# Kernel tuning notes

Hardware: AMD Instinct MI355X
Metric: run time of the kernel (lower is better)

Reference implementation:

```python
import jax, jax.numpy as jnp
import numpy as np

N_NODES = 100_000
N_EDGES = 800_000
HIDDEN = 150
EDGE_FEAT = 7
N_LAYERS = 4
N_GRAPHS = 128
OUT_DIM = 6
BN_EPS = 1e-5


def setup_inputs() -> dict:
    key = jax.random.key(0)
    ks = jax.random.split(key, 16)
    x = jnp.zeros((N_NODES,), dtype=jnp.int32)  # Embedding(1, D) -> all indices 0
    edge_index = jax.random.randint(ks[0], (2, N_EDGES), 0, N_NODES, dtype=jnp.int32)
    edge_attr = jax.random.normal(ks[1], (N_EDGES, EDGE_FEAT), dtype=jnp.float32)
    batch = jnp.sort(jax.random.randint(ks[2], (N_NODES,), 0, N_GRAPHS, dtype=jnp.int32))
    s = 0.05
    node_emb = jax.random.normal(ks[3], (1, HIDDEN), dtype=jnp.float32) * s
    Wl = jax.random.normal(ks[4], (N_LAYERS, HIDDEN, HIDDEN), dtype=jnp.float32) * s
    bl = jnp.zeros((N_LAYERS, HIDDEN), dtype=jnp.float32)
    We = jax.random.normal(ks[5], (N_LAYERS, EDGE_FEAT, HIDDEN), dtype=jnp.float32) * s
    be = jnp.zeros((N_LAYERS, HIDDEN), dtype=jnp.float32)
    root = jax.random.normal(ks[6], (N_LAYERS, 1, HIDDEN), dtype=jnp.float32) * s
    gamma = jnp.ones((N_LAYERS, HIDDEN), dtype=jnp.float32)
    beta = jnp.zeros((N_LAYERS, HIDDEN), dtype=jnp.float32)
    Wp = jax.random.normal(ks[7], (HIDDEN, OUT_DIM), dtype=jnp.float32) * s
    bp = jnp.zeros((OUT_DIM,), dtype=jnp.float32)
    return {"x": x, "edge_index": edge_index, "edge_attr": edge_attr, "batch": batch,
            "node_emb": node_emb, "Wl": Wl, "bl": bl, "We": We, "be": be,
            "root": root, "gamma": gamma, "beta": beta, "Wp": Wp, "bp": bp}


def reference(x, edge_index, edge_attr, batch, node_emb, Wl, bl, We, be, root, gamma, beta, Wp, bp):
    n = x.shape[0]
    row, col = edge_index[0], edge_index[1]  # j=source, i=target (PyG default flow)
    # degree over row (as in GCNConv.forward), +1
    deg = jax.ops.segment_sum(jnp.ones((row.shape[0],), edge_attr.dtype), row, num_segments=n) + 1.0
    dis = deg ** -0.5  # deg >= 1, no inf
    norm = dis[row] * dis[col]  # [E]

    h = node_emb[x]  # [N, D]
    for l in range(N_LAYERS):
        xl = h @ Wl[l] + bl[l]                      # linear
        e = edge_attr @ We[l] + be[l]               # edge encoder
        msg = norm[:, None] * jax.nn.relu(xl[row] + e)      # per-edge message [E, D]
        agg = jax.ops.segment_sum(msg, col, num_segments=n)  # scatter-add to targets
        out = agg + jax.nn.relu(xl + root[l]) / deg[:, None]
        # BatchNorm1d (training-mode batch statistics; dropout disabled = eval)
        mu = out.mean(axis=0)
        var = out.var(axis=0)
        out = gamma[l] * (out - mu) * jax.lax.rsqrt(var + BN_EPS) + beta[l]
        if l < N_LAYERS - 1:
            out = jax.nn.relu(out)
        h = out + h  # residual=True

    # global mean pool over graphs
    counts = jax.ops.segment_sum(jnp.ones((n,), h.dtype), batch, num_segments=N_GRAPHS)
    hg = jax.ops.segment_sum(h, batch, num_segments=N_GRAPHS) / jnp.maximum(counts, 1.0)[:, None]
    return hg @ Wp + bp  # [G, OUT_DIM]
```

## Files before the change

kernel.cpp:

```cpp
#include <hip/hip_runtime.h>

#define HID 150
#define LD  160
#define NN  100000
#define NNP 100096
#define NE  800000
#define NG  128
#define NL  4
#define ODIM 6
#define BN_EPS 1e-5f
#define NSLICE 32
#define NB_SCAN 98

typedef __attribute__((ext_vector_type(8))) short short8;
typedef __attribute__((ext_vector_type(4))) float f32x4;
typedef unsigned short ushort_t;

__device__ __forceinline__ unsigned short f2bf(float f) {
    union { float f; unsigned int u; } v; v.f = f;
    unsigned int u = v.u;
    unsigned int r = (u + 0x7FFFu + ((u >> 16) & 1u)) >> 16;
    return (unsigned short)r;
}
__device__ __forceinline__ float bf2f(unsigned short h) {
    union { unsigned int u; float f; } v; v.u = ((unsigned int)h) << 16;
    return v.f;
}

__global__ __launch_bounds__(256) void k_deg_count(const int* __restrict__ erow,
                                                   const int* __restrict__ ecol,
                                                   int* __restrict__ degi,
                                                   int* __restrict__ indeg) {
    int e = blockIdx.x * 256 + threadIdx.x;
    if (e < NE) {
        atomicAdd(&degi[erow[e]], 1);
        atomicAdd(&indeg[ecol[e]], 1);
    }
}

__global__ __launch_bounds__(256) void k_deg_fin(const int* __restrict__ degi,
                                                 float* __restrict__ degf,
                                                 float* __restrict__ dis) {
    int n = blockIdx.x * 256 + threadIdx.x;
    if (n < NN) {
        float dg = (float)degi[n] + 1.0f;
        degf[n] = dg;
        dis[n] = rsqrtf(dg);
    }
}

__global__ __launch_bounds__(1024) void k_scanA(const int* __restrict__ in,
                                                int* __restrict__ part,
                                                int* __restrict__ btot) {
    const int tid = threadIdx.x;
    const int lane = tid & 63, wave = tid >> 6;
    const int i = blockIdx.x * 1024 + tid;
    int v = (i < NN) ? in[i] : 0;
    int x = v;
#pragma unroll
    for (int o = 1; o < 64; o <<= 1) {
        int t = __shfl_up(x, o);
        if (lane >= o) x += t;
    }
    __shared__ int wsum[16];
    __shared__ int blocktot;
    if (lane == 63) wsum[wave] = x;
    __syncthreads();
    if (tid < 16) {
        int t = wsum[tid];
        int y = t;
#pragma unroll
        for (int o = 1; o < 16; o <<= 1) {
            int u = __shfl_up(y, o);
            if (tid >= o) y += u;
        }
        wsum[tid] = y - t;
        if (tid == 15) blocktot = y;
    }
    __syncthreads();
    int excl = x - v + wsum[wave];
    if (i < NN) part[i] = excl;
    if (tid == 0) btot[blockIdx.x] = blocktot;
}

__global__ __launch_bounds__(128) void k_scanB(int* __restrict__ btot) {
    const int tid = threadIdx.x;
    const int lane = tid & 63;
    int v = (tid < NB_SCAN) ? btot[tid] : 0;
    int x = v;
#pragma unroll
    for (int o = 1; o < 64; o <<= 1) {
        int t = __shfl_up(x, o);
        if (lane >= o) x += t;
    }
    __shared__ int w2;
    if (tid == 63) w2 = x;
    __syncthreads();
    int ex = x - v + ((tid >= 64) ? w2 : 0);
    if (tid < NB_SCAN) btot[tid] = ex;
}

__global__ __launch_bounds__(256) void k_scanC(int* __restrict__ coff,
                                               const int* __restrict__ btot,
                                               int* __restrict__ cursor) {
    int i = blockIdx.x * 256 + threadIdx.x;
    if (i < NN) {
        int v = coff[i] + btot[i >> 10];
        coff[i] = v;
        cursor[i] = v;
    }
    if (i == 0) coff[NN] = NE;
}

__global__ __launch_bounds__(256) void k_csr_fill(const int* __restrict__ erow,
                                                  const int* __restrict__ ecol,
                                                  const float* __restrict__ ea,
                                                  const float* __restrict__ dis,
                                                  int* __restrict__ cursor,
                                                  int2* __restrict__ csrn,
                                                  uint4* __restrict__ ceab) {
    int e = blockIdx.x * 256 + threadIdx.x;
    if (e >= NE) return;
    const int c = ecol[e], r = erow[e];
    const int p = atomicAdd(&cursor[c], 1);
    int2 m; m.x = r; m.y = __float_as_int(dis[r] * dis[c]);
    csrn[p] = m;
    const float a0 = ea[e * 7 + 0], a1 = ea[e * 7 + 1], a2 = ea[e * 7 + 2],
                a3 = ea[e * 7 + 3], a4 = ea[e * 7 + 4], a5 = ea[e * 7 + 5],
                a6 = ea[e * 7 + 6];
    uint4 A;
    A.x = (unsigned)f2bf(a0) | ((unsigned)f2bf(a1) << 16);
    A.y = (unsigned)f2bf(a2) | ((unsigned)f2bf(a3) << 16);
    A.z = (unsigned)f2bf(a4) | ((unsigned)f2bf(a5) << 16);
    A.w = (unsigned)f2bf(a6);
    ceab[p] = A;
}

__global__ __launch_bounds__(256) void k_wpack(const float* __restrict__ Wl,
                                               unsigned short* __restrict__ Wp) {
    int t = blockIdx.x * 256 + threadIdx.x;
    if (t >= 12800) return;
    const int lane = t & 63;
    const int ct = (t >> 6) % 10;
    const int ks = ((t >> 6) / 10) % 5;
    const int l = t / (64 * 10 * 5);
    const int col = ct * 16 + (lane & 15);
    const int kbase = ks * 32 + (lane >> 4) * 8;
    unsigned short v[8];
#pragma unroll
    for (int j = 0; j < 8; ++j) {
        const int k = kbase + j;
        const float f = (k < HID && col < HID) ? Wl[(size_t)l * HID * HID + k * HID + col] : 0.f;
        v[j] = f2bf(f);
    }
    *(uint4*)(Wp + (size_t)t * 8) = *(const uint4*)v;
}

__global__ __launch_bounds__(256) void k_init_h(const int* __restrict__ x,
                                                const float* __restrict__ emb,
                                                float* __restrict__ h,
                                                unsigned short* __restrict__ hb) {
    int idx = blockIdx.x * 256 + threadIdx.x;
    if (idx >= NNP * LD) return;
    int n = idx / LD;
    int d = idx - n * LD;
    float v = 0.f;
    if (n < NN && d < HID) v = emb[x[n] * HID + d];
    h[idx] = v;
    hb[idx] = f2bf(v);
}

__global__ __launch_bounds__(256) void k_gemm(const unsigned short* __restrict__ hb,
                                              const unsigned short* __restrict__ Wp,
                                              const float* __restrict__ bias,
                                              unsigned short* __restrict__ xlb) {
    __shared__ unsigned short Bs[5 * 10 * 64 * 8];
    {
        const uint4* src = (const uint4*)Wp;
        uint4* dst = (uint4*)Bs;
        for (int i = threadIdx.x; i < 3200; i += 256) dst[i] = src[i];
    }
    __syncthreads();

    const int wave = threadIdx.x >> 6;
    const int lane = threadIdx.x & 63;
    const int row0 = (blockIdx.x * 4 + wave) * 16;
    const int rlo = lane & 15;
    const int khi = lane >> 4;

    short8 a[5];
    {
        const unsigned short* ap = hb + (size_t)(row0 + rlo) * LD + khi * 8;
#pragma unroll
        for (int ks = 0; ks < 5; ++ks)
            a[ks] = *(const short8*)(ap + ks * 32);
    }

    f32x4 acc[10];
#pragma unroll
    for (int ct = 0; ct < 10; ++ct) acc[ct] = (f32x4){0.f, 0.f, 0.f, 0.f};

    const short8* bs = (const short8*)Bs;
#pragma unroll
    for (int ks = 0; ks < 5; ++ks) {
#pragma unroll
        for (int ct = 0; ct < 10; ++ct) {
            acc[ct] = __builtin_amdgcn_mfma_f32_16x16x32_bf16(
                a[ks], bs[(ks * 10 + ct) * 64 + lane], acc[ct], 0, 0, 0);
        }
    }

#pragma unroll
    for (int ct = 0; ct < 10; ++ct) {
        const int col = ct * 16 + rlo;
        if (col < HID) {
            const float b = bias[col];
#pragma unroll
            for (int jj = 0; jj < 4; ++jj) {
                const int row = row0 + khi * 4 + jj;
                xlb[(size_t)row * LD + col] = f2bf(acc[ct][jj] + b);
            }
        }
    }
}

__device__ __forceinline__ float edge_term(const uint4 A, const float w[8]) {
    float ed = w[7];
    ed = fmaf(bf2f((unsigned short)(A.x & 0xffffu)), w[0], ed);
    ed = fmaf(bf2f((unsigned short)(A.x >> 16)), w[1], ed);
    ed = fmaf(bf2f((unsigned short)(A.y & 0xffffu)), w[2], ed);
    ed = fmaf(bf2f((unsigned short)(A.y >> 16)), w[3], ed);
    ed = fmaf(bf2f((unsigned short)(A.z & 0xffffu)), w[4], ed);
    ed = fmaf(bf2f((unsigned short)(A.z >> 16)), w[5], ed);
    ed = fmaf(bf2f((unsigned short)(A.w & 0xffffu)), w[6], ed);
    return ed;
}

__global__ __launch_bounds__(256) void k_agg(const int* __restrict__ coff,
                                             const int2* __restrict__ csrn,
                                             const uint4* __restrict__ ceab,
                                             const float* __restrict__ We,
                                             const float* __restrict__ be,
                                             const float* __restrict__ root,
                                             const float* __restrict__ degf,
                                             const unsigned short* __restrict__ xlb,
                                             float* __restrict__ out,
                                             float* __restrict__ sums) {
    const int lane = threadIdx.x & 63;
    const int gw = (blockIdx.x * 256 + threadIdx.x) >> 6;
    const int nw = (gridDim.x * 256) >> 6;
    const bool ok2 = lane < (HID - 128);
    const int d0 = lane, d1 = lane + 64;
    const int d2 = ok2 ? (lane + 128) : 0;

    float w0[8], w1[8], w2[8];
    float rt0, rt1, rt2;
    {
        const int dd2 = ok2 ? (lane + 128) : 0;
#pragma unroll
        for (int k = 0; k < 7; ++k) {
            w0[k] = We[k * HID + d0];
            w1[k] = We[k * HID + d1];
            w2[k] = ok2 ? We[k * HID + dd2] : 0.f;
        }
        w0[7] = be[d0]; w1[7] = be[d1]; w2[7] = ok2 ? be[dd2] : 0.f;
        rt0 = root[d0]; rt1 = root[d1]; rt2 = ok2 ? root[dd2] : 0.f;
    }

    float s0 = 0.f, s1 = 0.f, s2 = 0.f, q0 = 0.f, q1 = 0.f, q2 = 0.f;

#define ACC_EDGE(m, A, xa, xb, xc)                                        \
    do {                                                                  \
        const float nrm = __int_as_float((m).y);                          \
        acc0 += nrm * fmaxf(bf2f(xa) + edge_term((A), w0), 0.f);          \
        acc1 += nrm * fmaxf(bf2f(xb) + edge_term((A), w1), 0.f);          \
        if (ok2) acc2 += nrm * fmaxf(bf2f(xc) + edge_term((A), w2), 0.f); \
    } while (0)

    for (int i = gw; i < NN; i += nw) {
        const int j1 = coff[i + 1];
        int j = coff[i];
        float acc0 = 0.f, acc1 = 0.f, acc2 = 0.f;
        for (; j + 4 <= j1; j += 4) {
            const int2 m0 = csrn[j], m1 = csrn[j + 1], m2 = csrn[j + 2], m3 = csrn[j + 3];
            const uint4 A0 = ceab[j], A1 = ceab[j + 1], A2 = ceab[j + 2], A3 = ceab[j + 3];
            const unsigned short* p0 = xlb + (size_t)m0.x * LD;
            const unsigned short* p1 = xlb + (size_t)m1.x * LD;
            const unsigned short* p2 = xlb + (size_t)m2.x * LD;
            const unsigned short* p3 = xlb + (size_t)m3.x * LD;
            const unsigned short x0a = p0[d0], x0b = p0[d1], x0c = p0[d2];
            const unsigned short x1a = p1[d0], x1b = p1[d1], x1c = p1[d2];
            const unsigned short x2a = p2[d0], x2b = p2[d1], x2c = p2[d2];
            const unsigned short x3a = p3[d0], x3b = p3[d1], x3c = p3[d2];
            ACC_EDGE(m0, A0, x0a, x0b, x0c);
            ACC_EDGE(m1, A1, x1a, x1b, x1c);
            ACC_EDGE(m2, A2, x2a, x2b, x2c);
            ACC_EDGE(m3, A3, x3a, x3b, x3c);
        }
        for (; j < j1; ++j) {
            const int2 m0 = csrn[j];
            const uint4 A0 = ceab[j];
            const unsigned short* p0 = xlb + (size_t)m0.x * LD;
            const unsigned short x0a = p0[d0], x0b = p0[d1], x0c = p0[d2];
            ACC_EDGE(m0, A0, x0a, x0b, x0c);
        }

        const float inv = 1.0f / degf[i];
        const unsigned short* xi = xlb + (size_t)i * LD;
        float* op = out + (size_t)i * LD;
        {
            const float o = acc0 + fmaxf(bf2f(xi[d0]) + rt0, 0.f) * inv;
            op[d0] = o; s0 += o; q0 += o * o;
        }
        {
            const float o = acc1 + fmaxf(bf2f(xi[d1]) + rt1, 0.f) * inv;
            op[d1] = o; s1 += o; q1 += o * o;
        }
        if (ok2) {
            const float o = acc2 + fmaxf(bf2f(xi[d2]) + rt2, 0.f) * inv;
            op[d2] = o; s2 += o; q2 += o * o;
        }
    }
#undef ACC_EDGE

    __shared__ float ls[2 * LD];
    for (int i = threadIdx.x; i < 2 * LD; i += 256) ls[i] = 0.f;
    __syncthreads();
    atomicAdd(&ls[d0], s0);
    atomicAdd(&ls[LD + d0], q0);
    atomicAdd(&ls[d1], s1);
    atomicAdd(&ls[LD + d1], q1);
    if (ok2) {
        atomicAdd(&ls[d2], s2);
        atomicAdd(&ls[LD + d2], q2);
    }
    __syncthreads();
    float* sl = sums + (size_t)(blockIdx.x & (NSLICE - 1)) * 2 * LD;
    for (int i = threadIdx.x; i < 2 * LD; i += 256) atomicAdd(&sl[i], ls[i]);
}

__global__ void k_stats(const float* __restrict__ sums, const float* __restrict__ gamma,
                        const float* __restrict__ beta, float* __restrict__ ss) {
    int d = threadIdx.x;
    if (d < HID) {
        float s = 0.f, q = 0.f;
        for (int r = 0; r < NSLICE; ++r) {
            s += sums[r * 2 * LD + d];
            q += sums[r * 2 * LD + LD + d];
        }
        const float mu = s * (1.0f / NN);
        const float var = q * (1.0f / NN) - mu * mu;
        const float inv = rsqrtf(var + BN_EPS);
        const float sc = gamma[d] * inv;
        ss[d] = sc;
        ss[LD + d] = beta[d] - mu * sc;
    }
}

__global__ __launch_bounds__(256) void k_apply(const float* __restrict__ out,
                                               const float* __restrict__ ss,
                                               float* __restrict__ h,
                                               unsigned short* __restrict__ hb,
                                               int doRelu) {
    const int lane = threadIdx.x & 63;
    const int gw = (blockIdx.x * 256 + threadIdx.x) >> 6;
    const int nw = (gridDim.x * 256) >> 6;
    const bool ok2 = lane < (HID - 128);

    float sc[3], sh[3];
#pragma unroll
    for (int c = 0; c < 3; ++c) {
        const int d = c * 64 + lane;
        const bool ok = (c < 2) || ok2;
        const int dd = ok ? d : 0;
        sc[c] = ok ? ss[dd] : 0.f;
        sh[c] = ok ? ss[LD + dd] : 0.f;
    }

    for (int n = gw; n < NN; n += nw) {
        float* hp = h + (size_t)n * LD;
        unsigned short* hbp = hb + (size_t)n * LD;
        const float* op = out + (size_t)n * LD;
#pragma unroll
        for (int c = 0; c < 3; ++c) {
            const int d = c * 64 + lane;
            if ((c < 2) || ok2) {
                float o = op[d] * sc[c] + sh[c];
                if (doRelu) o = fmaxf(o, 0.f);
                const float hn = hp[d] + o;
                hp[d] = hn;
                hbp[d] = f2bf(hn);
            }
        }
    }
}

__global__ __launch_bounds__(256) void k_off(const int* __restrict__ batch,
                                             int* __restrict__ off) {
    int n = blockIdx.x * 256 + threadIdx.x;
    if (n >= NN) return;
    int b = batch[n];
    if (n == 0) {
        for (int g = 0; g <= b; ++g) off[g] = 0;
    } else {
        int pb = batch[n - 1];
        for (int g = pb + 1; g <= b; ++g) off[g] = n;
    }
    if (n == NN - 1) {
        for (int g = b + 1; g <= NG; ++g) off[g] = NN;
    }
}

__global__ __launch_bounds__(256) void k_pool(const float* __restrict__ h,
                                              const int* __restrict__ off,
                                              const float* __restrict__ Wp,
                                              const float* __restrict__ bp,
                                              float* __restrict__ out) {
    const int g = blockIdx.x;
    const int s = off[g], e = off[g + 1];
    const float cnt = fmaxf((float)(e - s), 1.0f);
    const int lane = threadIdx.x & 63;
    const int wave = threadIdx.x >> 6;

    float sum[3] = {0.f, 0.f, 0.f};
    for (int n = s + wave; n < e; n += 4) {
        const float* hp = h + (size_t)n * LD;
#pragma unroll
        for (int c = 0; c < 3; ++c) {
            const int d = c * 64 + lane;
            if (d < HID) sum[c] += hp[d];
        }
    }

    __shared__ float hg[LD];
    if (threadIdx.x < LD) hg[threadIdx.x] = 0.f;
    __syncthreads();
#pragma unroll
    for (int c = 0; c < 3; ++c) {
        const int d = c * 64 + lane;
        if (d < HID) atomicAdd(&hg[d], sum[c]);
    }
    __syncthreads();

    if (wave == 0) {
        float acc[ODIM] = {0.f, 0.f, 0.f, 0.f, 0.f, 0.f};
#pragma unroll
        for (int c = 0; c < 3; ++c) {
            const int d = c * 64 + lane;
            if (d < HID) {
                const float v = hg[d] / cnt;
#pragma unroll
                for (int o = 0; o < ODIM; ++o) acc[o] = fmaf(v, Wp[d * ODIM + o], acc[o]);
            }
        }
#pragma unroll
        for (int o = 0; o < ODIM; ++o) {
            float v = acc[o];
            for (int sh = 32; sh > 0; sh >>= 1) v += __shfl_down(v, sh);
            if (lane == 0) out[g * ODIM + o] = v + bp[o];
        }
    }
}

extern "C" void kernel_launch(void* const* d_in, const int* in_sizes, int n_in,
                              void* d_out, int out_size, void* d_ws, size_t ws_size,
                              hipStream_t stream) {
    const int* x = (const int*)d_in[0];
    const int* ei = (const int*)d_in[1];
    const float* ea = (const float*)d_in[2];
    const int* batch = (const int*)d_in[3];
    const float* emb = (const float*)d_in[4];
    const float* Wl = (const float*)d_in[5];
    const float* bl = (const float*)d_in[6];
    const float* We = (const float*)d_in[7];
    const float* be = (const float*)d_in[8];
    const float* root = (const float*)d_in[9];
    const float* gamma = (const float*)d_in[10];
    const float* beta = (const float*)d_in[11];
    const float* Wp = (const float*)d_in[12];
    const float* bp = (const float*)d_in[13];
    float* out = (float*)d_out;

    const int* erow = ei;
    const int* ecol = ei + NE;

    char* ws = (char*)d_ws;
    const size_t SZ4 = (size_t)NNP * LD * 4;
    const size_t SZ2 = (size_t)NNP * LD * 2;
    float* h    = (float*)(ws);
    float* obuf = (float*)(ws + SZ4);
    unsigned short* hb  = (unsigned short*)(ws + 2 * SZ4);
    unsigned short* xlb = (unsigned short*)(ws + 2 * SZ4 + SZ2);
    unsigned short* wpk = (unsigned short*)(ws + 2 * SZ4 + 2 * SZ2);
    char* base = ws + 2 * SZ4 + 2 * SZ2 + 204800;
    int*   degi   = (int*)(base);
    int*   indeg  = (int*)(base + 409600);
    float* degf   = (float*)(base + 819200);
    float* dis    = (float*)(base + 1228800);
    int*   coff   = (int*)(base + 1638400);
    int*   cursor = (int*)(base + 2048000);
    int*   btot   = (int*)(base + 2457600);
    float* sums   = (float*)(base + 2461696);
    float* ssb    = (float*)(base + 2502656);
    int*   goff   = (int*)(base + 2506752);
    int2*  csrn   = (int2*)(base + 2510848);
    uint4* ceab   = (uint4*)(base + 8910848);

    hipMemsetAsync(degi, 0, NN * sizeof(int), stream);
    hipMemsetAsync(indeg, 0, NN * sizeof(int), stream);
    k_deg_count<<<(NE + 255) / 256, 256, 0, stream>>>(erow, ecol, degi, indeg);
    k_deg_fin<<<(NN + 255) / 256, 256, 0, stream>>>(degi, degf, dis);
    k_scanA<<<NB_SCAN, 1024, 0, stream>>>(indeg, coff, btot);
    k_scanB<<<1, 128, 0, stream>>>(btot);
    k_scanC<<<(NN + 255) / 256, 256, 0, stream>>>(coff, btot, cursor);
    k_csr_fill<<<(NE + 255) / 256, 256, 0, stream>>>(erow, ecol, ea, dis, cursor,
                                                     csrn, ceab);
    k_wpack<<<50, 256, 0, stream>>>(Wl, wpk);
    k_init_h<<<(NNP * LD + 255) / 256, 256, 0, stream>>>(x, emb, h, hb);

    for (int l = 0; l < NL; ++l) {
        const float* b_l = bl + (size_t)l * HID;
        const float* We_l = We + (size_t)l * 7 * HID;
        const float* be_l = be + (size_t)l * HID;
        const float* root_l = root + (size_t)l * HID;
        const float* gamma_l = gamma + (size_t)l * HID;
        const float* beta_l = beta + (size_t)l * HID;
        const unsigned short* wpk_l = wpk + (size_t)l * 25600;

        k_gemm<<<NNP / 64, 256, 0, stream>>>(hb, wpk_l, b_l, xlb);
        hipMemsetAsync(sums, 0, NSLICE * 2 * LD * sizeof(float), stream);
        k_agg<<<2048, 256, 0, stream>>>(coff, csrn, ceab, We_l, be_l,
                                        root_l, degf, xlb, obuf, sums);
        k_stats<<<1, 256, 0, stream>>>(sums, gamma_l, beta_l, ssb);
        k_apply<<<2048, 256, 0, stream>>>(obuf, ssb, h, hb, (l < NL - 1) ? 1 : 0);
    }

    k_off<<<(NN + 255) / 256, 256, 0, stream>>>(batch, goff);
    k_pool<<<NG, 256, 0, stream>>>(h, goff, Wp, bp, out);
}
```

Measured before the change: 996.8 us.

## Fuse BN apply and residual into next GEMM and pool; use bf16 dot2 for edge term

Removes the separate k_apply pass and the bf16 copy of h. The next layer's GEMM now reads obuf and h, applies the BN scale/shift, ReLU and residual, writes h back, and converts to bf16 in registers. The last layer's BN and residual are folded into the pooling kernel. The edge-encoder term in aggregation now uses packed bf16 weights with fdot2 instructions instead of seven scalar FMAs, which lowers the precision of the edge weights. The GEMM prologue now reads fp32 data (more bytes per row), and pooling runs with 512 threads.

```diff
diff --git a/kernel.cpp b/kernel.cpp
--- a/kernel.cpp
+++ b/kernel.cpp
@@ -14,7 +14,6 @@
 
 typedef __attribute__((ext_vector_type(8))) short short8;
 typedef __attribute__((ext_vector_type(4))) float f32x4;
-typedef unsigned short ushort_t;
 
 __device__ __forceinline__ unsigned short f2bf(float f) {
     union { float f; unsigned int u; } v; v.f = f;
@@ -25,6 +24,25 @@
 __device__ __forceinline__ float bf2f(unsigned short h) {
     union { unsigned int u; float f; } v; v.u = ((unsigned int)h) << 16;
     return v.f;
+}
+
+#if defined(__has_builtin)
+#if __has_builtin(__builtin_amdgcn_fdot2_f32_bf16)
+#define HAS_DOT2BF 1
+#endif
+#endif
+#ifdef HAS_DOT2BF
+typedef __attribute__((ext_vector_type(2))) __bf16 bf16x2;
+#endif
+__device__ __forceinline__ float dot2bf(unsigned int a, unsigned int b, float c) {
+#ifdef HAS_DOT2BF
+    union { unsigned int u; bf16x2 v; } ua, ub;
+    ua.u = a; ub.u = b;
+    return __builtin_amdgcn_fdot2_f32_bf16(ua.v, ub.v, c, false);
+#else
+    return fmaf(bf2f((unsigned short)(a & 0xffffu)), bf2f((unsigned short)(b & 0xffffu)),
+           fmaf(bf2f((unsigned short)(a >> 16)), bf2f((unsigned short)(b >> 16)), c));
+#endif
 }
 
 __global__ __launch_bounds__(256) void k_deg_count(const int* __restrict__ erow,
@@ -158,8 +176,7 @@
 
 __global__ __launch_bounds__(256) void k_init_h(const int* __restrict__ x,
                                                 const float* __restrict__ emb,
-                                                float* __restrict__ h,
-                                                unsigned short* __restrict__ hb) {
+                                                float* __restrict__ h) {
     int idx = blockIdx.x * 256 + threadIdx.x;
     if (idx >= NNP * LD) return;
     int n = idx / LD;
@@ -167,13 +184,15 @@
     float v = 0.f;
     if (n < NN && d < HID) v = emb[x[n] * HID + d];
     h[idx] = v;
-    hb[idx] = f2bf(v);
-}
-
-__global__ __launch_bounds__(256) void k_gemm(const unsigned short* __restrict__ hb,
+}
+
+__global__ __launch_bounds__(256) void k_gemm(float* __restrict__ h,
+                                              const float* __restrict__ obuf,
+                                              const float* __restrict__ ssb,
                                               const unsigned short* __restrict__ Wp,
                                               const float* __restrict__ bias,
-                                              unsigned short* __restrict__ xlb) {
+                                              unsigned short* __restrict__ xlb,
+                                              int fuse) {
     __shared__ unsigned short Bs[5 * 10 * 64 * 8];
     {
         const uint4* src = (const uint4*)Wp;
@@ -187,13 +206,58 @@
     const int row0 = (blockIdx.x * 4 + wave) * 16;
     const int rlo = lane & 15;
     const int khi = lane >> 4;
+    const int row = row0 + rlo;
+    const bool rowok = row < NN;
 
     short8 a[5];
-    {
-        const unsigned short* ap = hb + (size_t)(row0 + rlo) * LD + khi * 8;
-#pragma unroll
-        for (int ks = 0; ks < 5; ++ks)
-            a[ks] = *(const short8*)(ap + ks * 32);
+    if (fuse) {
+#pragma unroll
+        for (int ks = 0; ks < 5; ++ks) {
+            const int kf = ks * 32 + khi * 8;
+            const size_t base = (size_t)row * LD + kf;
+            const float4 o0 = *(const float4*)(obuf + base);
+            const float4 o1 = *(const float4*)(obuf + base + 4);
+            const float4 h0 = *(const float4*)(h + base);
+            const float4 h1 = *(const float4*)(h + base + 4);
+            const float4 s0 = *(const float4*)(ssb + kf);
+            const float4 s1 = *(const float4*)(ssb + kf + 4);
+            const float4 t0 = *(const float4*)(ssb + LD + kf);
+            const float4 t1 = *(const float4*)(ssb + LD + kf + 4);
+            float hv[8];
+#pragma unroll
+            for (int j = 0; j < 4; ++j) {
+                const bool ok = rowok && (kf + j < HID);
+                hv[j] = ok ? ((&h0.x)[j] + fmaxf((&o0.x)[j] * (&s0.x)[j] + (&t0.x)[j], 0.f)) : 0.f;
+            }
+#pragma unroll
+            for (int j = 0; j < 4; ++j) {
+                const bool ok = rowok && (kf + 4 + j < HID);
+                hv[4 + j] = ok ? ((&h1.x)[j] + fmaxf((&o1.x)[j] * (&s1.x)[j] + (&t1.x)[j], 0.f)) : 0.f;
+            }
+            float4 w0, w1;
+            w0.x = hv[0]; w0.y = hv[1]; w0.z = hv[2]; w0.w = hv[3];
+            w1.x = hv[4]; w1.y = hv[5]; w1.z = hv[6]; w1.w = hv[7];
+            *(float4*)(h + base) = w0;
+            *(float4*)(h + base + 4) = w1;
+            short8 av;
+#pragma unroll
+            for (int j = 0; j < 8; ++j) av[j] = (short)f2bf(hv[j]);
+            a[ks] = av;
+        }
+    } else {
+#pragma unroll
+        for (int ks = 0; ks < 5; ++ks) {
+            const int kf = ks * 32 + khi * 8;
+            const size_t base = (size_t)row * LD + kf;
+            const float4 h0 = *(const float4*)(h + base);
+            const float4 h1 = *(const float4*)(h + base + 4);
+            short8 av;
+#pragma unroll
+            for (int j = 0; j < 4; ++j) av[j] = (short)f2bf((&h0.x)[j]);
+#pragma unroll
+            for (int j = 0; j < 4; ++j) av[4 + j] = (short)f2bf((&h1.x)[j]);
+            a[ks] = av;
+        }
     }
 
     f32x4 acc[10];
@@ -217,23 +281,11 @@
             const float b = bias[col];
 #pragma unroll
             for (int jj = 0; jj < 4; ++jj) {
-                const int row = row0 + khi * 4 + jj;
-                xlb[(size_t)row * LD + col] = f2bf(acc[ct][jj] + b);
+                const int orow = row0 + khi * 4 + jj;
+                xlb[(size_t)orow * LD + col] = f2bf(acc[ct][jj] + b);
             }
         }
     }
-}
-
-__device__ __forceinline__ float edge_term(const uint4 A, const float w[8]) {
-    float ed = w[7];
-    ed = fmaf(bf2f((unsigned short)(A.x & 0xffffu)), w[0], ed);
-    ed = fmaf(bf2f((unsigned short)(A.x >> 16)), w[1], ed);
-    ed = fmaf(bf2f((unsigned short)(A.y & 0xffffu)), w[2], ed);
-    ed = fmaf(bf2f((unsigned short)(A.y >> 16)), w[3], ed);
-    ed = fmaf(bf2f((unsigned short)(A.z & 0xffffu)), w[4], ed);
-    ed = fmaf(bf2f((unsigned short)(A.z >> 16)), w[5], ed);
-    ed = fmaf(bf2f((unsigned short)(A.w & 0xffffu)), w[6], ed);
-    return ed;
 }
 
 __global__ __launch_bounds__(256) void k_agg(const int* __restrict__ coff,
@@ -253,28 +305,38 @@
     const int d0 = lane, d1 = lane + 64;
     const int d2 = ok2 ? (lane + 128) : 0;
 
-    float w0[8], w1[8], w2[8];
-    float rt0, rt1, rt2;
+    unsigned int wp0[4], wp1[4], wp2[4];
+    float be0, be1, be2, rt0, rt1, rt2;
     {
-        const int dd2 = ok2 ? (lane + 128) : 0;
-#pragma unroll
-        for (int k = 0; k < 7; ++k) {
-            w0[k] = We[k * HID + d0];
-            w1[k] = We[k * HID + d1];
-            w2[k] = ok2 ? We[k * HID + dd2] : 0.f;
-        }
-        w0[7] = be[d0]; w1[7] = be[d1]; w2[7] = ok2 ? be[dd2] : 0.f;
-        rt0 = root[d0]; rt1 = root[d1]; rt2 = ok2 ? root[dd2] : 0.f;
+#pragma unroll
+        for (int p = 0; p < 3; ++p) {
+            wp0[p] = (unsigned)f2bf(We[(2 * p) * HID + d0]) | ((unsigned)f2bf(We[(2 * p + 1) * HID + d0]) << 16);
+            wp1[p] = (unsigned)f2bf(We[(2 * p) * HID + d1]) | ((unsigned)f2bf(We[(2 * p + 1) * HID + d1]) << 16);
+            wp2[p] = ok2 ? ((unsigned)f2bf(We[(2 * p) * HID + d2]) | ((unsigned)f2bf(We[(2 * p + 1) * HID + d2]) << 16)) : 0u;
+        }
+        wp0[3] = (unsigned)f2bf(We[6 * HID + d0]);
+        wp1[3] = (unsigned)f2bf(We[6 * HID + d1]);
+        wp2[3] = ok2 ? (unsigned)f2bf(We[6 * HID + d2]) : 0u;
+        be0 = be[d0]; be1 = be[d1]; be2 = ok2 ? be[d2] : 0.f;
+        rt0 = root[d0]; rt1 = root[d1]; rt2 = ok2 ? root[d2] : 0.f;
     }
 
     float s0 = 0.f, s1 = 0.f, s2 = 0.f, q0 = 0.f, q1 = 0.f, q2 = 0.f;
 
-#define ACC_EDGE(m, A, xa, xb, xc)                                        \
-    do {                                                                  \
-        const float nrm = __int_as_float((m).y);                          \
-        acc0 += nrm * fmaxf(bf2f(xa) + edge_term((A), w0), 0.f);          \
-        acc1 += nrm * fmaxf(bf2f(xb) + edge_term((A), w1), 0.f);          \
-        if (ok2) acc2 += nrm * fmaxf(bf2f(xc) + edge_term((A), w2), 0.f); \
+#define ACC_EDGE(m, A, xa, xb, xc)                                                          \
+    do {                                                                                    \
+        const float nrm = __int_as_float((m).y);                                            \
+        const float e0 = dot2bf((A).x, wp0[0], dot2bf((A).y, wp0[1],                        \
+                         dot2bf((A).z, wp0[2], dot2bf((A).w, wp0[3], be0))));               \
+        const float e1 = dot2bf((A).x, wp1[0], dot2bf((A).y, wp1[1],                        \
+                         dot2bf((A).z, wp1[2], dot2bf((A).w, wp1[3], be1))));               \
+        acc0 += nrm * fmaxf(bf2f(xa) + e0, 0.f);                                            \
+        acc1 += nrm * fmaxf(bf2f(xb) + e1, 0.f);                                            \
+        if (ok2) {                                                                          \
+            const float e2 = dot2bf((A).x, wp2[0], dot2bf((A).y, wp2[1],                    \
+                             dot2bf((A).z, wp2[2], dot2bf((A).w, wp2[3], be2))));           \
+            acc2 += nrm * fmaxf(bf2f(xc) + e2, 0.f);                                        \
+        }                                                                                   \
     } while (0)
 
     for (int i = gw; i < NN; i += nw) {
@@ -354,44 +416,9 @@
         const float sc = gamma[d] * inv;
         ss[d] = sc;
         ss[LD + d] = beta[d] - mu * sc;
-    }
-}
-
-__global__ __launch_bounds__(256) void k_apply(const float* __restrict__ out,
-                                               const float* __restrict__ ss,
-                                               float* __restrict__ h,
-                                               unsigned short* __restrict__ hb,
-                                               int doRelu) {
-    const int lane = threadIdx.x & 63;
-    const int gw = (blockIdx.x * 256 + threadIdx.x) >> 6;
-    const int nw = (gridDim.x * 256) >> 6;
-    const bool ok2 = lane < (HID - 128);
-
-    float sc[3], sh[3];
-#pragma unroll
-    for (int c = 0; c < 3; ++c) {
-        const int d = c * 64 + lane;
-        const bool ok = (c < 2) || ok2;
-        const int dd = ok ? d : 0;
-        sc[c] = ok ? ss[dd] : 0.f;
-        sh[c] = ok ? ss[LD + dd] : 0.f;
-    }
-
-    for (int n = gw; n < NN; n += nw) {
-        float* hp = h + (size_t)n * LD;
-        unsigned short* hbp = hb + (size_t)n * LD;
-        const float* op = out + (size_t)n * LD;
-#pragma unroll
-        for (int c = 0; c < 3; ++c) {
-            const int d = c * 64 + lane;
-            if ((c < 2) || ok2) {
-                float o = op[d] * sc[c] + sh[c];
-                if (doRelu) o = fmaxf(o, 0.f);
-                const float hn = hp[d] + o;
-                hp[d] = hn;
-                hbp[d] = f2bf(hn);
-            }
-        }
+    } else if (d < LD) {
+        ss[d] = 0.f;
+        ss[LD + d] = 0.f;
     }
 }
 
@@ -411,7 +438,9 @@
     }
 }
 
-__global__ __launch_bounds__(256) void k_pool(const float* __restrict__ h,
+__global__ __launch_bounds__(512) void k_pool(const float* __restrict__ h,
+                                              const float* __restrict__ obuf,
+                                              const float* __restrict__ ssb,
                                               const int* __restrict__ off,
                                               const float* __restrict__ Wp,
                                               const float* __restrict__ bp,
@@ -421,25 +450,28 @@
     const float cnt = fmaxf((float)(e - s), 1.0f);
     const int lane = threadIdx.x & 63;
     const int wave = threadIdx.x >> 6;
-
-    float sum[3] = {0.f, 0.f, 0.f};
-    for (int n = s + wave; n < e; n += 4) {
+    const bool ok2 = lane < (HID - 128);
+    const int d0 = lane, d1 = lane + 64;
+    const int d2 = ok2 ? (lane + 128) : 0;
+
+    const float sc0 = ssb[d0], sc1 = ssb[d1], sc2 = ok2 ? ssb[d2] : 0.f;
+    const float sh0 = ssb[LD + d0], sh1 = ssb[LD + d1], sh2 = ok2 ? ssb[LD + d2] : 0.f;
+
+    float sum0 = 0.f, sum1 = 0.f, sum2 = 0.f;
+    for (int n = s + wave; n < e; n += 8) {
         const float* hp = h + (size_t)n * LD;
-#pragma unroll
-        for (int c = 0; c < 3; ++c) {
-            const int d = c * 64 + lane;
-            if (d < HID) sum[c] += hp[d];
-        }
+        const float* op = obuf + (size_t)n * LD;
+        sum0 += hp[d0] + (op[d0] * sc0 + sh0);
+        sum1 += hp[d1] + (op[d1] * sc1 + sh1);
+        if (ok2) sum2 += hp[d2] + (op[d2] * sc2 + sh2);
     }
 
     __shared__ float hg[LD];
     if (threadIdx.x < LD) hg[threadIdx.x] = 0.f;
     __syncthreads();
-#pragma unroll
-    for (int c = 0; c < 3; ++c) {
-        const int d = c * 64 + lane;
-        if (d < HID) atomicAdd(&hg[d], sum[c]);
-    }
+    atomicAdd(&hg[d0], sum0);
+    atomicAdd(&hg[d1], sum1);
+    if (ok2) atomicAdd(&hg[d2], sum2);
     __syncthreads();
 
     if (wave == 0) {
@@ -489,10 +521,9 @@
     const size_t SZ2 = (size_t)NNP * LD * 2;
     float* h    = (float*)(ws);
     float* obuf = (float*)(ws + SZ4);
-    unsigned short* hb  = (unsigned short*)(ws + 2 * SZ4);
-    unsigned short* xlb = (unsigned short*)(ws + 2 * SZ4 + SZ2);
-    unsigned short* wpk = (unsigned short*)(ws + 2 * SZ4 + 2 * SZ2);
-    char* base = ws + 2 * SZ4 + 2 * SZ2 + 204800;
+    unsigned short* xlb = (unsigned short*)(ws + 2 * SZ4);
+    unsigned short* wpk = (unsigned short*)(ws + 2 * SZ4 + SZ2);
+    char* base = ws + 2 * SZ4 + SZ2 + 204800;
     int*   degi   = (int*)(base);
     int*   indeg  = (int*)(base + 409600);
     float* degf   = (float*)(base + 819200);
@@ -516,7 +547,7 @@
     k_csr_fill<<<(NE + 255) / 256, 256, 0, stream>>>(erow, ecol, ea, dis, cursor,
                                                      csrn, ceab);
     k_wpack<<<50, 256, 0, stream>>>(Wl, wpk);
-    k_init_h<<<(NNP * LD + 255) / 256, 256, 0, stream>>>(x, emb, h, hb);
+    k_init_h<<<(NNP * LD + 255) / 256, 256, 0, stream>>>(x, emb, h);
 
     for (int l = 0; l < NL; ++l) {
         const float* b_l = bl + (size_t)l * HID;
@@ -527,14 +558,14 @@
         const float* beta_l = beta + (size_t)l * HID;
         const unsigned short* wpk_l = wpk + (size_t)l * 25600;
 
-        k_gemm<<<NNP / 64, 256, 0, stream>>>(hb, wpk_l, b_l, xlb);
+        k_gemm<<<NNP / 64, 256, 0, stream>>>(h, obuf, ssb, wpk_l, b_l, xlb,
+                                             (l > 0) ? 1 : 0);
         hipMemsetAsync(sums, 0, NSLICE * 2 * LD * sizeof(float), stream);
         k_agg<<<2048, 256, 0, stream>>>(coff, csrn, ceab, We_l, be_l,
                                         root_l, degf, xlb, obuf, sums);
         k_stats<<<1, 256, 0, stream>>>(sums, gamma_l, beta_l, ssb);
-        k_apply<<<2048, 256, 0, stream>>>(obuf, ssb, h, hb, (l < NL - 1) ? 1 : 0);
     }
 
     k_off<<<(NN + 255) / 256, 256, 0, stream>>>(batch, goff);
-    k_pool<<<NG, 256, 0, stream>>>(h, goff, Wp, bp, out);
-}
+    k_pool<<<NG, 512, 0, stream>>>(h, obuf, ssb, goff, Wp, bp, out);
+}
```

After: 903.8 us. 1.1x faster.
